# Kernel tuning notes

Hardware: AMD Instinct MI355X
Metric: run time of the kernel (lower is better)

## Reference

```python
import jax, jax.numpy as jnp
import numpy as np

H, N, CH, RANK = 512, 64, 1, 1
SEQ_L = 4096


def setup_inputs() -> dict:
    key = jax.random.key(0)
    k0, k1, k2, k3, k4 = jax.random.split(key, 5)
    # A = -exp(A_real) + i*A_imag  (real_transform='exp'); HiPPO-style imag init
    A_real = jnp.log(0.5 + jax.random.uniform(k0, (H, N), dtype=jnp.float32))
    A_imag = jnp.broadcast_to(np.pi * jnp.arange(N, dtype=jnp.float32), (H, N)).copy()
    # complex params stored as (..., 2) real/imag pairs (torch.view_as_real layout)
    B = (0.5 ** 0.5) * jax.random.normal(k1, (1, H, N, 2), dtype=jnp.float32)
    C = jax.random.normal(k2, (CH, H, N, 2), dtype=jnp.float32)
    P = (0.5 ** 0.5) * jax.random.normal(k3, (RANK, H, N, 2), dtype=jnp.float32)
    # dt = exp(inv_dt) log-uniform in [1e-3, 1e-1]  (dt_transform='exp')
    lo, hi = np.log(1e-3), np.log(1e-1)
    inv_dt = (lo + (hi - lo) * jax.random.uniform(k4, (H,), dtype=jnp.float32)).astype(jnp.float32)
    return {"A_real": A_real, "A_imag": A_imag, "B": B, "C": C, "P": P,
            "inv_dt": inv_dt, "L": SEQ_L}


def _c(x):
    # view_as_complex
    return x[..., 0] + 1j * x[..., 1]


def _s4_kernel(A_real, A_imag, B, C, P, inv_dt, L):
    dt = jnp.exp(inv_dt)                       # (H,)
    A = -jnp.exp(A_real) + 1j * A_imag          # (H, N) complex64
    Bc, Cc, Pc = _c(B), _c(C), _c(P)            # (1,H,N), (CH,H,N), (R,H,N)
    Q = jnp.conj(Pc)

    Lf = L // 2 + 1
    omega = jnp.exp(-2j * jnp.pi / L) ** jnp.arange(Lf)   # FFT nodes, (Lf,)
    z = 2 * (1 - omega) / (1 + omega)                      # bilinear-transform freqs

    A_dt = A * dt[:, None]                     # (H, N)
    Bcat = jnp.concatenate([Bc, Pc], axis=0)   # (1+R, H, N)
    Ccat = jnp.concatenate([Cc, Q], axis=0)    # (CH+R, H, N)
    v = Bcat[:, None] * Ccat[None]             # (1+R, CH+R, H, N)
    v = v * dt[:, None]

    # Cauchy kernel with implicit conjugate-pair symmetry:
    #   r[a,b,h,l] = sum_n v/(z - A_dt) + conj(v)/(z - conj(A_dt))
    denom = 1.0 / (z - A_dt[..., None])                    # (H, N, Lf)
    r = jnp.einsum('abhn,hnl->abhl', v, denom)
    denom_c = 1.0 / (z - jnp.conj(A_dt)[..., None])
    r = r + jnp.einsum('abhn,hnl->abhl', jnp.conj(v), denom_c)

    # rank-1 Woodbury correction
    k_f = r[:-1, :-1] - r[:-1, -1:] * r[-1:, :-1] / (1 + r[-1:, -1:])
    k_f = k_f * 2 / (1 + omega)

    k = jnp.fft.irfft(k_f, n=L)                # (1, CH, H, L) real
    k = k[..., :L]
    return k[-1]                               # k_B: (CH, H, L)


def reference(A_real, A_imag, B, C, P, inv_dt, L):
    return _s4_kernel(A_real, A_imag, B, C, P, inv_dt, L)
```

## Files before the change

kernel.cpp:

```cpp
#include <hip/hip_runtime.h>
#include <math.h>

namespace {
constexpr int kH = 512;
constexpr int kN = 64;
constexpr int kL = 4096;
constexpr int kM = 2048;
constexpr int kPairRec = 40;
constexpr int kThreads = 256;
constexpr int kFftThreads = 512;
constexpr float kPi = 3.14159265358979323846f;
}

typedef float v2f __attribute__((ext_vector_type(2)));

__device__ __forceinline__ int lpad(int i) { return i + (i >> 4); }
__device__ __forceinline__ v2f fma2(v2f a, v2f b, v2f c) {
    return __builtin_elementwise_fma(a, b, c);
}
__device__ __forceinline__ float2 cmul(float2 a, float2 b) {
    return make_float2(a.x*b.x - a.y*b.y, a.x*b.y + a.y*b.x);
}

__global__ __launch_bounds__(64)
void s4_prep(const float* __restrict__ A_real, const float* __restrict__ A_imag,
             const float* __restrict__ Bv, const float* __restrict__ Cv,
             const float* __restrict__ Pv, const float* __restrict__ inv_dt,
             float* __restrict__ cst, float* __restrict__ xnyq)
{
    const int h = blockIdx.x;
    const int n = threadIdx.x;
    const int idx = h * kN + n;
    const float dt = expf(inv_dt[h]);
    const float ar = -expf(A_real[idx]) * dt;
    const float ai =  A_imag[idx] * dt;
    const float br = Bv[idx*2+0], bi = Bv[idx*2+1];
    const float cr = Cv[idx*2+0], ci = Cv[idx*2+1];
    const float pr = Pv[idx*2+0], pi = Pv[idx*2+1];
    const float v00r = (br*cr - bi*ci)*dt, v00i = (br*ci + bi*cr)*dt;
    const float v01r = (br*pr + bi*pi)*dt, v01i = (bi*pr - br*pi)*dt;
    const float v10r = (pr*cr - pi*ci)*dt, v10i = (pr*ci + pi*cr)*dt;
    const float v11r = (pr*pr + pi*pi)*dt;
    const float ar2 = ar*ar;
    const float C1  = ar2 + ai*ai;
    const float dd  = ar2 - ai*ai;

    float co[16];
    co[0]  = -2.f*C1*(v00r*ar + v00i*ai);   co[1]  = 2.f*(v00i*ai - v00r*ar);
    co[2]  = -4.f*v00r*dd - 8.f*v00i*ar*ai; co[3]  = -4.f*v00r;
    co[4]  = -2.f*C1*(v01r*ar + v01i*ai);   co[5]  = 2.f*(v01i*ai - v01r*ar);
    co[6]  = -4.f*v01r*dd - 8.f*v01i*ar*ai; co[7]  = -4.f*v01r;
    co[8]  = -2.f*C1*(v10r*ar + v10i*ai);   co[9]  = 2.f*(v10i*ai - v10r*ar);
    co[10] = -4.f*v10r*dd - 8.f*v10i*ar*ai; co[11] = -4.f*v10r;
    co[12] = -2.f*C1*(v11r*ar);             co[13] = -2.f*v11r*ar;
    co[14] = -4.f*v11r*dd;                  co[15] = -4.f*v11r;

    float* base = cst + ((size_t)h * (kN/2) + (n >> 1)) * kPairRec + (n & 1);
    base[0] = ai;
    base[2] = ar2;
    #pragma unroll
    for (int k = 0; k < 16; ++k) base[4 + 2*k] = co[k];

    float s = v00r;
    #pragma unroll
    for (int off = 32; off > 0; off >>= 1) s += __shfl_down(s, off, 64);
    if (n == 0) xnyq[h] = s;
}

__global__ __launch_bounds__(kThreads)
void s4_spectrum(const float* __restrict__ cst, float2* __restrict__ Xg)
{
    const int b   = blockIdx.x;
    const int h   = (b & 7) + 8 * ((b >> 3) & 63);
    const int q   = b >> 9;
    const int tid = threadIdx.x;
    const int la  = q * 512 + tid;

    float tvb[2], svb[2];
    v2f t2p[2];
    #pragma unroll
    for (int bb = 0; bb < 2; ++bb) {
        const int l = la + 256 * bb;
        float sn, cn;
        sincosf((float)l * (kPi / (float)kL), &sn, &cn);
        tvb[bb] = sn / cn;
        const float t2 = 2.f * tvb[bb];
        svb[bb] = t2 * t2;
        t2p[bb] = (v2f){t2, t2};
    }

    v2f A0[2][4], A1[2][4], B0[2][4], B1[2][4];
    #pragma unroll
    for (int bb = 0; bb < 2; ++bb)
        #pragma unroll
        for (int p = 0; p < 4; ++p) {
            A0[bb][p] = (v2f){0.f, 0.f}; A1[bb][p] = (v2f){0.f, 0.f};
            B0[bb][p] = (v2f){0.f, 0.f}; B1[bb][p] = (v2f){0.f, 0.f};
        }

    const v2f* rec = (const v2f*)(cst + (size_t)h * (kN/2) * kPairRec);
    #pragma unroll 2
    for (int j = 0; j < kN/2; ++j) {
        const v2f* r = rec + j * (kPairRec/2);
        const v2f aip  = r[0];
        const v2f ar2p = r[1];
        #pragma unroll
        for (int bb = 0; bb < 2; ++bb) {
            const v2f w1 = t2p[bb] - aip;
            const v2f w2 = t2p[bb] + aip;
            const v2f m1 = fma2(w1, w1, ar2p);
            const v2f m2 = fma2(w2, w2, ar2p);
            const v2f D  = m1 * m2;
            const float qq = __builtin_amdgcn_rcpf(D.x * D.y);
            v2f qv;
            qv.x = D.y * qq;
            qv.y = D.x * qq;
            #pragma unroll
            for (int p = 0; p < 4; ++p) {
                A0[bb][p] = fma2(r[2 + 4*p + 0], qv, A0[bb][p]);
                A1[bb][p] = fma2(r[2 + 4*p + 1], qv, A1[bb][p]);
                B0[bb][p] = fma2(r[2 + 4*p + 2], qv, B0[bb][p]);
                B1[bb][p] = fma2(r[2 + 4*p + 3], qv, B1[bb][p]);
            }
        }
    }

    #pragma unroll
    for (int bb = 0; bb < 2; ++bb) {
        const int l = la + 256 * bb;
        const float t = tvb[bb];
        const v2f sp = (v2f){svb[bb], svb[bb]};
        const v2f r00 = fma2(sp, A1[bb][0], A0[bb][0]);
        const v2f i00 = fma2(sp, B1[bb][0], B0[bb][0]);
        const v2f r01 = fma2(sp, A1[bb][1], A0[bb][1]);
        const v2f i01 = fma2(sp, B1[bb][1], B0[bb][1]);
        const v2f r10 = fma2(sp, A1[bb][2], A0[bb][2]);
        const v2f i10 = fma2(sp, B1[bb][2], B0[bb][2]);
        const v2f r11 = fma2(sp, A1[bb][3], A0[bb][3]);
        const v2f i11 = fma2(sp, B1[bb][3], B0[bb][3]);
        const float s00r = r00.x + r00.y, s00i = t * (i00.x + i00.y);
        const float s01r = r01.x + r01.y, s01i = t * (i01.x + i01.y);
        const float s10r = r10.x + r10.y, s10i = t * (i10.x + i10.y);
        const float s11r = r11.x + r11.y, s11i = t * (i11.x + i11.y);
        const float nr = s01r*s10r - s01i*s10i;
        const float ni = s01r*s10i + s01i*s10r;
        const float dr = 1.f + s11r, di = s11i;
        const float qd = __builtin_amdgcn_rcpf(fmaf(dr, dr, di*di));
        const float wr = (nr*dr + ni*di) * qd;
        const float wi = (ni*dr - nr*di) * qd;
        const float gr = s00r - wr, gi = s00i - wi;
        Xg[h*kM + l] = make_float2(fmaf(-gi, t, gr), fmaf(gr, t, gi));
    }
}

__global__ __launch_bounds__(kFftThreads)
void s4_ifft(const float* __restrict__ xnyq, float* __restrict__ out)
{
    __shared__ float2 W2[kM + kM / 16];
    __shared__ float2 TW[kM / 2 + kM / 32];

    const int h   = blockIdx.x;
    const int tid = threadIdx.x;
    const float2* Xg = (const float2*)(out + (size_t)h * kL);
    const float nyqR = xnyq[h];

    for (int j = tid; j < kM / 2; j += kFftThreads) {
        float s, c;
        sincosf((2.0f * kPi / (float)kM) * (float)j, &s, &c);
        TW[lpad(j)] = make_float2(c, s);
    }

    for (int k = tid; k <= kM / 2; k += kFftThreads) {
        const float2 Xa = Xg[k];
        const float2 Xb = (k == 0) ? make_float2(nyqR, 0.0f) : Xg[kM - k];
        const float Er = 0.5f * (Xa.x + Xb.x);
        const float Ei = 0.5f * (Xa.y - Xb.y);
        const float Dr = 0.5f * (Xa.x - Xb.x);
        const float Di = 0.5f * (Xa.y + Xb.y);
        float s, c;
        sincosf((2.0f * kPi / (float)kL) * (float)k, &s, &c);
        const float Or = c * Dr - s * Di;
        const float Oi = c * Di + s * Dr;
        const int rk = (int)(__brev((unsigned)k) >> 21);
        W2[lpad(rk)] = make_float2(Er - Oi, Ei + Or);
        if (k != 0 && k != kM / 2) {
            const int rmk = (int)(__brev((unsigned)(kM - k)) >> 21);
            W2[lpad(rmk)] = make_float2(Er + Oi, Or - Ei);
        }
    }
    __syncthreads();

    for (int j = tid; j < kM / 4; j += kFftThreads) {
        const int i0 = j * 4;
        const float2 e0 = W2[lpad(i0)];
        const float2 e1 = W2[lpad(i0 + 1)];
        const float2 e2 = W2[lpad(i0 + 2)];
        const float2 e3 = W2[lpad(i0 + 3)];
        const float2 a0 = make_float2(e0.x + e1.x, e0.y + e1.y);
        const float2 a1 = make_float2(e0.x - e1.x, e0.y - e1.y);
        const float2 a2 = make_float2(e2.x + e3.x, e2.y + e3.y);
        const float2 a3 = make_float2(e2.x - e3.x, e2.y - e3.y);
        W2[lpad(i0)]     = make_float2(a0.x + a2.x, a0.y + a2.y);
        W2[lpad(i0 + 2)] = make_float2(a0.x - a2.x, a0.y - a2.y);
        W2[lpad(i0 + 1)] = make_float2(a1.x - a3.y, a1.y + a3.x);
        W2[lpad(i0 + 3)] = make_float2(a1.x + a3.y, a1.y - a3.x);
    }
    __syncthreads();

    #pragma unroll
    for (int lg = 2; lg <= 8; lg += 2) {
        const int hs = 1 << lg;
        const int twstride = 512 >> lg;
        for (int j = tid; j < kM / 4; j += kFftThreads) {
            const int pos = j & (hs - 1);
            const int grp = j >> lg;
            const int i0  = grp * 4 * hs + pos;
            const float2 e0 = W2[lpad(i0)];
            const float2 e1 = W2[lpad(i0 + hs)];
            const float2 e2 = W2[lpad(i0 + 2*hs)];
            const float2 e3 = W2[lpad(i0 + 3*hs)];
            const float2 wB = TW[lpad(pos * twstride)];
            const float2 wA = cmul(wB, wB);
            const float2 t1 = cmul(wA, e1);
            const float2 t3 = cmul(wA, e3);
            const float2 a0 = make_float2(e0.x + t1.x, e0.y + t1.y);
            const float2 a1 = make_float2(e0.x - t1.x, e0.y - t1.y);
            const float2 a2 = make_float2(e2.x + t3.x, e2.y + t3.y);
            const float2 a3 = make_float2(e2.x - t3.x, e2.y - t3.y);
            const float2 u2 = cmul(wB, a2);
            const float2 u3 = cmul(wB, a3);
            W2[lpad(i0)]        = make_float2(a0.x + u2.x, a0.y + u2.y);
            W2[lpad(i0 + 2*hs)] = make_float2(a0.x - u2.x, a0.y - u2.y);
            W2[lpad(i0 + hs)]   = make_float2(a1.x - u3.y, a1.y + u3.x);
            W2[lpad(i0 + 3*hs)] = make_float2(a1.x + u3.y, a1.y - u3.x);
        }
        __syncthreads();
    }
    for (int j = tid; j < kM / 2; j += kFftThreads) {
        const float2 tw = TW[lpad(j)];
        const float2 a  = W2[lpad(j)];
        const float2 b  = W2[lpad(j + 1024)];
        const float2 tb = cmul(tw, b);
        W2[lpad(j)]        = make_float2(a.x + tb.x, a.y + tb.y);
        W2[lpad(j + 1024)] = make_float2(a.x - tb.x, a.y - tb.y);
    }
    __syncthreads();

    const float invM = 1.0f / (float)kM;
    float2* out2 = (float2*)(out + (size_t)h * kL);
    for (int n = tid; n < kM; n += kFftThreads) {
        const float2 zn = W2[lpad(n)];
        out2[n] = make_float2(zn.x * invM, zn.y * invM);
    }
}

extern "C" void kernel_launch(void* const* d_in, const int* in_sizes, int n_in,
                              void* d_out, int out_size, void* d_ws, size_t ws_size,
                              hipStream_t stream) {
    const float* A_real = (const float*)d_in[0];
    const float* A_imag = (const float*)d_in[1];
    const float* B      = (const float*)d_in[2];
    const float* C      = (const float*)d_in[3];
    const float* P      = (const float*)d_in[4];
    const float* inv_dt = (const float*)d_in[5];
    float* out = (float*)d_out;

    float* cst  = (float*)d_ws;
    float* xnyq = cst + (size_t)kH * (kN/2) * kPairRec;

    s4_prep<<<dim3(kH), dim3(64), 0, stream>>>(A_real, A_imag, B, C, P, inv_dt,
                                               cst, xnyq);
    s4_spectrum<<<dim3(kH * 4), dim3(kThreads), 0, stream>>>(cst, (float2*)out);
    s4_ifft<<<dim3(kH), dim3(kFftThreads), 0, stream>>>(xnyq, out);
}
```

Baseline: 106.7 us.

## Fuse Cauchy spectrum evaluation and inverse FFT into one per-head kernel

```diff
diff --git a/kernel.cpp b/kernel.cpp
--- a/kernel.cpp
+++ b/kernel.cpp
@@ -7,8 +7,7 @@
 constexpr int kL = 4096;
 constexpr int kM = 2048;
 constexpr int kPairRec = 40;
-constexpr int kThreads = 256;
-constexpr int kFftThreads = 512;
+constexpr int kFusedThreads = 512;
 constexpr float kPi = 3.14159265358979323846f;
 }
 
@@ -67,112 +66,109 @@
     if (n == 0) xnyq[h] = s;
 }
 
-__global__ __launch_bounds__(kThreads)
-void s4_spectrum(const float* __restrict__ cst, float2* __restrict__ Xg)
+__global__ __launch_bounds__(kFusedThreads)
+void s4_spec_ifft(const float* __restrict__ cst, const float* __restrict__ xnyq,
+                  float* __restrict__ out)
 {
-    const int b   = blockIdx.x;
-    const int h   = (b & 7) + 8 * ((b >> 3) & 63);
-    const int q   = b >> 9;
-    const int tid = threadIdx.x;
-    const int la  = q * 512 + tid;
-
-    float tvb[2], svb[2];
-    v2f t2p[2];
-    #pragma unroll
-    for (int bb = 0; bb < 2; ++bb) {
-        const int l = la + 256 * bb;
-        float sn, cn;
-        sincosf((float)l * (kPi / (float)kL), &sn, &cn);
-        tvb[bb] = sn / cn;
-        const float t2 = 2.f * tvb[bb];
-        svb[bb] = t2 * t2;
-        t2p[bb] = (v2f){t2, t2};
-    }
-
-    v2f A0[2][4], A1[2][4], B0[2][4], B1[2][4];
-    #pragma unroll
-    for (int bb = 0; bb < 2; ++bb)
-        #pragma unroll
-        for (int p = 0; p < 4; ++p) {
-            A0[bb][p] = (v2f){0.f, 0.f}; A1[bb][p] = (v2f){0.f, 0.f};
-            B0[bb][p] = (v2f){0.f, 0.f}; B1[bb][p] = (v2f){0.f, 0.f};
-        }
-
-    const v2f* rec = (const v2f*)(cst + (size_t)h * (kN/2) * kPairRec);
-    #pragma unroll 2
-    for (int j = 0; j < kN/2; ++j) {
-        const v2f* r = rec + j * (kPairRec/2);
-        const v2f aip  = r[0];
-        const v2f ar2p = r[1];
-        #pragma unroll
-        for (int bb = 0; bb < 2; ++bb) {
-            const v2f w1 = t2p[bb] - aip;
-            const v2f w2 = t2p[bb] + aip;
-            const v2f m1 = fma2(w1, w1, ar2p);
-            const v2f m2 = fma2(w2, w2, ar2p);
-            const v2f D  = m1 * m2;
-            const float qq = __builtin_amdgcn_rcpf(D.x * D.y);
-            v2f qv;
-            qv.x = D.y * qq;
-            qv.y = D.x * qq;
-            #pragma unroll
-            for (int p = 0; p < 4; ++p) {
-                A0[bb][p] = fma2(r[2 + 4*p + 0], qv, A0[bb][p]);
-                A1[bb][p] = fma2(r[2 + 4*p + 1], qv, A1[bb][p]);
-                B0[bb][p] = fma2(r[2 + 4*p + 2], qv, B0[bb][p]);
-                B1[bb][p] = fma2(r[2 + 4*p + 3], qv, B1[bb][p]);
-            }
-        }
-    }
-
-    #pragma unroll
-    for (int bb = 0; bb < 2; ++bb) {
-        const int l = la + 256 * bb;
-        const float t = tvb[bb];
-        const v2f sp = (v2f){svb[bb], svb[bb]};
-        const v2f r00 = fma2(sp, A1[bb][0], A0[bb][0]);
-        const v2f i00 = fma2(sp, B1[bb][0], B0[bb][0]);
-        const v2f r01 = fma2(sp, A1[bb][1], A0[bb][1]);
-        const v2f i01 = fma2(sp, B1[bb][1], B0[bb][1]);
-        const v2f r10 = fma2(sp, A1[bb][2], A0[bb][2]);
-        const v2f i10 = fma2(sp, B1[bb][2], B0[bb][2]);
-        const v2f r11 = fma2(sp, A1[bb][3], A0[bb][3]);
-        const v2f i11 = fma2(sp, B1[bb][3], B0[bb][3]);
-        const float s00r = r00.x + r00.y, s00i = t * (i00.x + i00.y);
-        const float s01r = r01.x + r01.y, s01i = t * (i01.x + i01.y);
-        const float s10r = r10.x + r10.y, s10i = t * (i10.x + i10.y);
-        const float s11r = r11.x + r11.y, s11i = t * (i11.x + i11.y);
-        const float nr = s01r*s10r - s01i*s10i;
-        const float ni = s01r*s10i + s01i*s10r;
-        const float dr = 1.f + s11r, di = s11i;
-        const float qd = __builtin_amdgcn_rcpf(fmaf(dr, dr, di*di));
-        const float wr = (nr*dr + ni*di) * qd;
-        const float wi = (ni*dr - nr*di) * qd;
-        const float gr = s00r - wr, gi = s00i - wi;
-        Xg[h*kM + l] = make_float2(fmaf(-gi, t, gr), fmaf(gr, t, gi));
-    }
-}
-
-__global__ __launch_bounds__(kFftThreads)
-void s4_ifft(const float* __restrict__ xnyq, float* __restrict__ out)
-{
+    __shared__ float2 XS[kM];
     __shared__ float2 W2[kM + kM / 16];
     __shared__ float2 TW[kM / 2 + kM / 32];
 
     const int h   = blockIdx.x;
     const int tid = threadIdx.x;
-    const float2* Xg = (const float2*)(out + (size_t)h * kL);
-    const float nyqR = xnyq[h];
-
-    for (int j = tid; j < kM / 2; j += kFftThreads) {
+
+    for (int j = tid; j < kM / 2; j += kFusedThreads) {
         float s, c;
         sincosf((2.0f * kPi / (float)kM) * (float)j, &s, &c);
         TW[lpad(j)] = make_float2(c, s);
     }
 
-    for (int k = tid; k <= kM / 2; k += kFftThreads) {
-        const float2 Xa = Xg[k];
-        const float2 Xb = (k == 0) ? make_float2(nyqR, 0.0f) : Xg[kM - k];
+    const v2f* rec = (const v2f*)(cst + (size_t)h * (kN/2) * kPairRec);
+    #pragma unroll 1
+    for (int pass = 0; pass < 2; ++pass) {
+        const int la = pass * 1024 + tid;
+
+        float tvb[2], svb[2];
+        v2f t2p[2];
+        #pragma unroll
+        for (int bb = 0; bb < 2; ++bb) {
+            const int l = la + 512 * bb;
+            float sn, cn;
+            sincosf((float)l * (kPi / (float)kL), &sn, &cn);
+            tvb[bb] = sn / cn;
+            const float t2 = 2.f * tvb[bb];
+            svb[bb] = t2 * t2;
+            t2p[bb] = (v2f){t2, t2};
+        }
+
+        v2f A0[2][4], A1[2][4], B0[2][4], B1[2][4];
+        #pragma unroll
+        for (int bb = 0; bb < 2; ++bb)
+            #pragma unroll
+            for (int p = 0; p < 4; ++p) {
+                A0[bb][p] = (v2f){0.f, 0.f}; A1[bb][p] = (v2f){0.f, 0.f};
+                B0[bb][p] = (v2f){0.f, 0.f}; B1[bb][p] = (v2f){0.f, 0.f};
+            }
+
+        #pragma unroll 2
+        for (int j = 0; j < kN/2; ++j) {
+            const v2f* r = rec + j * (kPairRec/2);
+            const v2f aip  = r[0];
+            const v2f ar2p = r[1];
+            #pragma unroll
+            for (int bb = 0; bb < 2; ++bb) {
+                const v2f w1 = t2p[bb] - aip;
+                const v2f w2 = t2p[bb] + aip;
+                const v2f m1 = fma2(w1, w1, ar2p);
+                const v2f m2 = fma2(w2, w2, ar2p);
+                const v2f D  = m1 * m2;
+                const float qq = __builtin_amdgcn_rcpf(D.x * D.y);
+                v2f qv;
+                qv.x = D.y * qq;
+                qv.y = D.x * qq;
+                #pragma unroll
+                for (int p = 0; p < 4; ++p) {
+                    A0[bb][p] = fma2(r[2 + 4*p + 0], qv, A0[bb][p]);
+                    A1[bb][p] = fma2(r[2 + 4*p + 1], qv, A1[bb][p]);
+                    B0[bb][p] = fma2(r[2 + 4*p + 2], qv, B0[bb][p]);
+                    B1[bb][p] = fma2(r[2 + 4*p + 3], qv, B1[bb][p]);
+                }
+            }
+        }
+
+        #pragma unroll
+        for (int bb = 0; bb < 2; ++bb) {
+            const int l = la + 512 * bb;
+            const float t = tvb[bb];
+            const v2f sp = (v2f){svb[bb], svb[bb]};
+            const v2f r00 = fma2(sp, A1[bb][0], A0[bb][0]);
+            const v2f i00 = fma2(sp, B1[bb][0], B0[bb][0]);
+            const v2f r01 = fma2(sp, A1[bb][1], A0[bb][1]);
+            const v2f i01 = fma2(sp, B1[bb][1], B0[bb][1]);
+            const v2f r10 = fma2(sp, A1[bb][2], A0[bb][2]);
+            const v2f i10 = fma2(sp, B1[bb][2], B0[bb][2]);
+            const v2f r11 = fma2(sp, A1[bb][3], A0[bb][3]);
+            const v2f i11 = fma2(sp, B1[bb][3], B0[bb][3]);
+            const float s00r = r00.x + r00.y, s00i = t * (i00.x + i00.y);
+            const float s01r = r01.x + r01.y, s01i = t * (i01.x + i01.y);
+            const float s10r = r10.x + r10.y, s10i = t * (i10.x + i10.y);
+            const float s11r = r11.x + r11.y, s11i = t * (i11.x + i11.y);
+            const float nr = s01r*s10r - s01i*s10i;
+            const float ni = s01r*s10i + s01i*s10r;
+            const float dr = 1.f + s11r, di = s11i;
+            const float qd = __builtin_amdgcn_rcpf(fmaf(dr, dr, di*di));
+            const float wr = (nr*dr + ni*di) * qd;
+            const float wi = (ni*dr - nr*di) * qd;
+            const float gr = s00r - wr, gi = s00i - wi;
+            XS[l] = make_float2(fmaf(-gi, t, gr), fmaf(gr, t, gi));
+        }
+    }
+    __syncthreads();
+
+    const float nyqR = xnyq[h];
+    for (int k = tid; k <= kM / 2; k += kFusedThreads) {
+        const float2 Xa = XS[k];
+        const float2 Xb = (k == 0) ? make_float2(nyqR, 0.0f) : XS[kM - k];
         const float Er = 0.5f * (Xa.x + Xb.x);
         const float Ei = 0.5f * (Xa.y - Xb.y);
         const float Dr = 0.5f * (Xa.x - Xb.x);
@@ -190,7 +186,7 @@
     }
     __syncthreads();
 
-    for (int j = tid; j < kM / 4; j += kFftThreads) {
+    for (int j = tid; j < kM / 4; j += kFusedThreads) {
         const int i0 = j * 4;
         const float2 e0 = W2[lpad(i0)];
         const float2 e1 = W2[lpad(i0 + 1)];
@@ -211,7 +207,7 @@
     for (int lg = 2; lg <= 8; lg += 2) {
         const int hs = 1 << lg;
         const int twstride = 512 >> lg;
-        for (int j = tid; j < kM / 4; j += kFftThreads) {
+        for (int j = tid; j < kM / 4; j += kFusedThreads) {
             const int pos = j & (hs - 1);
             const int grp = j >> lg;
             const int i0  = grp * 4 * hs + pos;
@@ -236,7 +232,7 @@
         }
         __syncthreads();
     }
-    for (int j = tid; j < kM / 2; j += kFftThreads) {
+    for (int j = tid; j < kM / 2; j += kFusedThreads) {
         const float2 tw = TW[lpad(j)];
         const float2 a  = W2[lpad(j)];
         const float2 b  = W2[lpad(j + 1024)];
@@ -248,7 +244,7 @@
 
     const float invM = 1.0f / (float)kM;
     float2* out2 = (float2*)(out + (size_t)h * kL);
-    for (int n = tid; n < kM; n += kFftThreads) {
+    for (int n = tid; n < kM; n += kFusedThreads) {
         const float2 zn = W2[lpad(n)];
         out2[n] = make_float2(zn.x * invM, zn.y * invM);
     }
@@ -270,6 +266,5 @@
 
     s4_prep<<<dim3(kH), dim3(64), 0, stream>>>(A_real, A_imag, B, C, P, inv_dt,
                                                cst, xnyq);
-    s4_spectrum<<<dim3(kH * 4), dim3(kThreads), 0, stream>>>(cst, (float2*)out);
-    s4_ifft<<<dim3(kH), dim3(kFftThreads), 0, stream>>>(xnyq, out);
-}
+    s4_spec_ifft<<<dim3(kH), dim3(kFusedThreads), 0, stream>>>(cst, xnyq, out);
+}
```

Measured after the change: 106.2 us. About the same (-0.5%).
